# Kernel tuning notes

Hardware: AMD Instinct MI355X
Metric: run time of the kernel (lower is better)

The kernel has to match this reference:

```python
import jax, jax.numpy as jnp
import numpy as np

BS, N, XC, K, YS = 64, 1024, 1024, 256, 768

def setup_inputs() -> dict:
    key = jax.random.key(0)
    ks = jax.random.split(key, 5)
    return {
        "x": jax.random.normal(ks[0], (BS, N, XC), dtype=jnp.float32),
        "y": jax.random.normal(ks[1], (BS, YS), dtype=jnp.float32),
        "W_ch": jax.random.normal(ks[2], (K, XC), dtype=jnp.float32) * 0.02,
        "b_ch": jax.random.normal(ks[3], (K,), dtype=jnp.float32) * 0.02,
        "W_y": jax.random.normal(ks[4], (K, YS), dtype=jnp.float32) * 0.02,
    }

def reference(x, y, W_ch, b_ch, W_y):
    # y_k: [bs, k] (no bias)
    y_k = jnp.einsum('bs,ks->bk', y, W_y)
    # channel affine on every spatial position, batched: [bs, n, k]
    x_k = jnp.einsum('bnc,kc->bnk', x, W_ch) + b_ch
    # add per-sample y_k (broadcast over spatial dim), tanh, softmax over k
    z = jnp.tanh(x_k + y_k[:, None, :])
    attn = jax.nn.softmax(z, axis=-1)
    # torch.cat over dim=0 of per-sample [n, k] blocks -> [bs*n, k]
    return attn.reshape(-1, attn.shape[-1])
```

## Files before the change

kernel.cpp:

```cpp
#include <hip/hip_runtime.h>


#define XC    1024
#define KOUT  256
#define NT    16
#define LDSZ  16384

typedef float        f32x4_t  __attribute__((ext_vector_type(4)));
typedef unsigned int u32x4_t  __attribute__((ext_vector_type(4)));
typedef unsigned int u32x2_t  __attribute__((ext_vector_type(2)));
typedef __bf16       bf16x8_t __attribute__((ext_vector_type(8)));

__device__ __forceinline__ unsigned short f2bf(float f) {
  unsigned int u = __float_as_uint(f);
  u += 0x7fffu + ((u >> 16) & 1u);
  return (unsigned short)(u >> 16);
}

__device__ __forceinline__ float fast_tanh(float v) {
  float e = __expf(2.0f * v);
  return 1.0f - 2.0f / (e + 1.0f);
}

#define LGKM_BARRIER() do {                                  \
    asm volatile("s_waitcnt lgkmcnt(0)" ::: "memory");       \
    __builtin_amdgcn_s_barrier();                            \
    __builtin_amdgcn_sched_barrier(0);                       \
  } while (0)

__global__ void prep_kernel(const float* __restrict__ Wch,
                            const float* __restrict__ y,
                            const float* __restrict__ Wy,
                            const float* __restrict__ bch,
                            unsigned short* __restrict__ wbf,
                            float* __restrict__ biasws) {
  if (blockIdx.x < 256) {
    const int k = blockIdx.x;
    const int u = threadIdx.x;
    f32x4_t v = ((const f32x4_t*)(Wch + k * XC))[u];
    const int c0   = u << 2;
    const int t    = c0 >> 6;
    const int ch   = (c0 & 63) >> 3;
    const int kk   = ch >> 2;
    const int lg   = ch & 3;
    const int half = (c0 >> 2) & 1;
    const int wv   = k >> 6;
    const int ni   = (k >> 4) & 3;
    const int lr   = k & 15;
    const int lane = (lg << 4) | lr;
    unsigned int lo = (unsigned int)f2bf(v.x) | ((unsigned int)f2bf(v.y) << 16);
    unsigned int hi = (unsigned int)f2bf(v.z) | ((unsigned int)f2bf(v.w) << 16);
    char* p = (char*)wbf +
              ((size_t)((((t << 2) + wv) * 2 + kk) * 4 + ni) << 10) +
              (lane << 4) + (half << 3);
    *(u32x2_t*)p = (u32x2_t){lo, hi};
  } else {
    __shared__ __align__(16) float ys[768];
    const int b = blockIdx.x - 256;
    const int k = threadIdx.x;
    for (int i = k; i < 768; i += 256) ys[i] = y[b * 768 + i];
    __syncthreads();
    const f32x4_t* w4 = (const f32x4_t*)(Wy + k * 768);
    const f32x4_t* y4 = (const f32x4_t*)ys;
    float s = 0.f;
#pragma unroll 8
    for (int i = 0; i < 192; ++i) {
      f32x4_t w = w4[i], a = y4[i];
      s = fmaf(w.x, a.x, s); s = fmaf(w.y, a.y, s);
      s = fmaf(w.z, a.z, s); s = fmaf(w.w, a.w, s);
    }
    biasws[b * 256 + k] = s + bch[k];
  }
}

__global__ __launch_bounds__(256, 2) void fused_kernel(
    const float* __restrict__ x, const unsigned short* __restrict__ wbf,
    const float* __restrict__ bias, float* __restrict__ out) {
  __shared__ __align__(16) unsigned char smem[LDSZ];
  const int tid = threadIdx.x;
  const int l   = tid & 63;
  const int wv  = tid >> 6;
  const int lr  = l & 15;
  const int lg  = l >> 4;
  const int m0  = blockIdx.x << 6;
  const int bidx = m0 >> 10;
  const int rr  = tid >> 4;
  const int c4  = tid & 15;

  f32x4_t acc[4][4];
#pragma unroll
  for (int i = 0; i < 4; ++i)
#pragma unroll
    for (int j = 0; j < 4; ++j) acc[i][j] = (f32x4_t){0.f, 0.f, 0.f, 0.f};

  const float* xb = x + (size_t)m0 * XC + (size_t)rr * XC + (c4 << 2);
  const char* wsrc = (const char*)wbf;
  f32x4_t avA[4], avB[4];
  bf16x8_t bfr[8];

#define LOADA(dst, tt) do {                                                  \
    _Pragma("unroll")                                                        \
    for (int j = 0; j < 4; ++j)                                              \
      dst[j] = *(const f32x4_t*)(xb + (size_t)(j << 4) * XC + ((tt) << 6));  \
  } while (0)

#define LOADB(tt) do {                                                       \
    const char* g = wsrc + (size_t)(tt) * 32768 + (wv << 13) + (l << 4);     \
    _Pragma("unroll")                                                        \
    for (int f = 0; f < 8; ++f)                                              \
      bfr[f] = __builtin_bit_cast(bf16x8_t, *(const u32x4_t*)(g + (f << 10)));\
  } while (0)

#define WRITEA(src, buf) do {                                                \
    _Pragma("unroll")                                                        \
    for (int j = 0; j < 4; ++j) {                                            \
      const int row = (j << 4) + rr;                                         \
      unsigned int lo = (unsigned int)f2bf(src[j].x) |                       \
                        ((unsigned int)f2bf(src[j].y) << 16);                \
      unsigned int hi = (unsigned int)f2bf(src[j].z) |                       \
                        ((unsigned int)f2bf(src[j].w) << 16);                \
      char* p = (char*)smem + ((buf) << 13) + row * 128 +                    \
                (((c4 >> 1) ^ (row & 7)) << 4) + ((c4 & 1) << 3);            \
      *(u32x2_t*)p = (u32x2_t){lo, hi};                                      \
    }                                                                        \
  } while (0)

#define COMPUTE(buf) do {                                                    \
    const u32x4_t* aB = (const u32x4_t*)(smem + ((buf) << 13));              \
    _Pragma("unroll")                                                        \
    for (int kk = 0; kk < 2; ++kk) {                                         \
      const int cs = ((kk << 2) | lg) ^ (lr & 7);                            \
      bf16x8_t afr[4];                                                       \
      _Pragma("unroll")                                                      \
      for (int mi = 0; mi < 4; ++mi)                                         \
        afr[mi] = __builtin_bit_cast(bf16x8_t, aB[(((mi << 4) + lr) << 3) + cs]);\
      _Pragma("unroll")                                                      \
      for (int mi = 0; mi < 4; ++mi)                                         \
        _Pragma("unroll")                                                    \
        for (int nj = 0; nj < 4; ++nj)                                       \
          acc[mi][nj] = __builtin_amdgcn_mfma_f32_16x16x32_bf16(             \
              afr[mi], bfr[(kk << 2) | nj], acc[mi][nj], 0, 0, 0);           \
    }                                                                        \
  } while (0)

  LOADA(avA, 0);
  LOADA(avB, 1);
  LOADB(0);
  WRITEA(avA, 0);
  LGKM_BARRIER();

  for (int t = 0; t < NT; t += 2) {
    if (t + 2 < NT) LOADA(avA, t + 2);
    COMPUTE(0);
    if (t + 1 < NT) LOADB(t + 1);
    if (t + 1 < NT) WRITEA(avB, 1);
    LGKM_BARRIER();
    if (t + 3 < NT) LOADA(avB, t + 3);
    COMPUTE(1);
    if (t + 2 < NT) LOADB(t + 2);
    if (t + 2 < NT) WRITEA(avA, 0);
    if (t + 2 < NT) LGKM_BARRIER();
  }
  __syncthreads();

#undef LOADA
#undef LOADB
#undef WRITEA
#undef COMPUTE

  float* wred    = (float*)smem;
  float* rowstat = (float*)(smem + 1024);

  float brow[4];
#pragma unroll
  for (int ni = 0; ni < 4; ++ni)
    brow[ni] = bias[(bidx << 8) + (wv << 6) + (ni << 4) + lr];

#pragma unroll
  for (int mi = 0; mi < 4; ++mi)
#pragma unroll
    for (int ni = 0; ni < 4; ++ni)
#pragma unroll
      for (int r = 0; r < 4; ++r)
        acc[mi][ni][r] = fast_tanh(acc[mi][ni][r] + brow[ni]);

#pragma unroll
  for (int mi = 0; mi < 4; ++mi)
#pragma unroll
    for (int r = 0; r < 4; ++r) {
      float m = fmaxf(fmaxf(acc[mi][0][r], acc[mi][1][r]),
                      fmaxf(acc[mi][2][r], acc[mi][3][r]));
      m = fmaxf(m, __shfl_xor(m, 1));
      m = fmaxf(m, __shfl_xor(m, 2));
      m = fmaxf(m, __shfl_xor(m, 4));
      m = fmaxf(m, __shfl_xor(m, 8));
      if (lr == 0) wred[(wv << 6) + (mi << 4) + (lg << 2) + r] = m;
    }
  __syncthreads();
  if (tid < 64)
    rowstat[tid] = fmaxf(fmaxf(wred[tid], wred[64 + tid]),
                         fmaxf(wred[128 + tid], wred[192 + tid]));
  __syncthreads();

#pragma unroll
  for (int mi = 0; mi < 4; ++mi)
#pragma unroll
    for (int r = 0; r < 4; ++r) {
      const int row = (mi << 4) + (lg << 2) + r;
      const float m = rowstat[row];
      float s = 0.f;
#pragma unroll
      for (int ni = 0; ni < 4; ++ni) {
        float e = __expf(acc[mi][ni][r] - m);
        acc[mi][ni][r] = e;
        s += e;
      }
      s += __shfl_xor(s, 1);
      s += __shfl_xor(s, 2);
      s += __shfl_xor(s, 4);
      s += __shfl_xor(s, 8);
      if (lr == 0) wred[(wv << 6) + row] = s;
    }
  __syncthreads();
  if (tid < 64)
    rowstat[tid] = 1.0f / (wred[tid] + wred[64 + tid] +
                           wred[128 + tid] + wred[192 + tid]);
  __syncthreads();

#pragma unroll
  for (int mi = 0; mi < 4; ++mi)
#pragma unroll
    for (int r = 0; r < 4; ++r) {
      const int row = (mi << 4) + (lg << 2) + r;
      const float rinv = rowstat[row];
      float* orow = out + (size_t)(m0 + row) * KOUT + (wv << 6) + lr;
#pragma unroll
      for (int ni = 0; ni < 4; ++ni)
        orow[ni << 4] = acc[mi][ni][r] * rinv;
    }
}

extern "C" void kernel_launch(void* const* d_in, const int* in_sizes, int n_in,
                              void* d_out, int out_size, void* d_ws, size_t ws_size,
                              hipStream_t stream) {
  (void)in_sizes; (void)n_in; (void)out_size; (void)ws_size;
  const float* x   = (const float*)d_in[0];
  const float* y   = (const float*)d_in[1];
  const float* Wch = (const float*)d_in[2];
  const float* bch = (const float*)d_in[3];
  const float* Wy  = (const float*)d_in[4];
  float* out = (float*)d_out;
  unsigned short* wbf = (unsigned short*)d_ws;
  float* biasws = (float*)((char*)d_ws + 512 * 1024);

  hipLaunchKernelGGL(prep_kernel, dim3(320), dim3(256), 0, stream,
                     Wch, y, Wy, bch, wbf, biasws);
  hipLaunchKernelGGL(fused_kernel, dim3(1024), dim3(256), 0, stream,
                     x, wbf, biasws, out);
}
```

Baseline: 117.5 us.

## Stage weight tiles into LDS via async global_load_lds with triple-buffered A

```diff
diff --git a/kernel.cpp b/kernel.cpp
--- a/kernel.cpp
+++ b/kernel.cpp
@@ -4,7 +4,8 @@
 #define XC    1024
 #define KOUT  256
 #define NT    16
-#define LDSZ  16384
+#define B_OFF 16384
+#define LDSZ  81920
 
 typedef float        f32x4_t  __attribute__((ext_vector_type(4)));
 typedef unsigned int u32x4_t  __attribute__((ext_vector_type(4)));
@@ -17,16 +18,24 @@
   return (unsigned short)(u >> 16);
 }
 
+__device__ __forceinline__ unsigned int pack2bf(float a, float b) {
+  unsigned int ua = __float_as_uint(a) + 0x8000u;
+  unsigned int ub = __float_as_uint(b) + 0x8000u;
+  return (ua >> 16) | (ub & 0xffff0000u);
+}
+
 __device__ __forceinline__ float fast_tanh(float v) {
   float e = __expf(2.0f * v);
   return 1.0f - 2.0f / (e + 1.0f);
 }
 
-#define LGKM_BARRIER() do {                                  \
-    asm volatile("s_waitcnt lgkmcnt(0)" ::: "memory");       \
-    __builtin_amdgcn_s_barrier();                            \
-    __builtin_amdgcn_sched_barrier(0);                       \
-  } while (0)
+__device__ __forceinline__ void async_copy16(void* lds, const void* g) {
+  __builtin_amdgcn_global_load_lds(
+      (const __attribute__((address_space(1))) void*)g,
+      (__attribute__((address_space(3))) void*)lds, 16, 0, 0);
+}
+
+#define PIPE_WAIT(N) asm volatile("s_waitcnt vmcnt(" #N ")" ::: "memory")
 
 __global__ void prep_kernel(const float* __restrict__ Wch,
                             const float* __restrict__ y,
@@ -86,6 +95,7 @@
   const int bidx = m0 >> 10;
   const int rr  = tid >> 4;
   const int c4  = tid & 15;
+  const int t0  = blockIdx.x & 15;
 
   f32x4_t acc[4][4];
 #pragma unroll
@@ -95,8 +105,7 @@
 
   const float* xb = x + (size_t)m0 * XC + (size_t)rr * XC + (c4 << 2);
   const char* wsrc = (const char*)wbf;
-  f32x4_t avA[4], avB[4];
-  bf16x8_t bfr[8];
+  f32x4_t av0[4], av1[4], av2[4];
 
 #define LOADA(dst, tt) do {                                                  \
     _Pragma("unroll")                                                        \
@@ -104,21 +113,20 @@
       dst[j] = *(const f32x4_t*)(xb + (size_t)(j << 4) * XC + ((tt) << 6));  \
   } while (0)
 
-#define LOADB(tt) do {                                                       \
+#define DMAB(tt, buf) do {                                                   \
     const char* g = wsrc + (size_t)(tt) * 32768 + (wv << 13) + (l << 4);     \
-    _Pragma("unroll")                                                        \
-    for (int f = 0; f < 8; ++f)                                              \
-      bfr[f] = __builtin_bit_cast(bf16x8_t, *(const u32x4_t*)(g + (f << 10)));\
+    unsigned char* d = smem + B_OFF + ((buf) << 15) + (wv << 13);            \
+    _Pragma("unroll")                                                        \
+    for (int i = 0; i < 8; ++i)                                              \
+      async_copy16(d + (i << 10), g + (i << 10));                            \
   } while (0)
 
 #define WRITEA(src, buf) do {                                                \
     _Pragma("unroll")                                                        \
     for (int j = 0; j < 4; ++j) {                                            \
       const int row = (j << 4) + rr;                                         \
-      unsigned int lo = (unsigned int)f2bf(src[j].x) |                       \
-                        ((unsigned int)f2bf(src[j].y) << 16);                \
-      unsigned int hi = (unsigned int)f2bf(src[j].z) |                       \
-                        ((unsigned int)f2bf(src[j].w) << 16);                \
+      unsigned int lo = pack2bf(src[j].x, src[j].y);                         \
+      unsigned int hi = pack2bf(src[j].z, src[j].w);                         \
       char* p = (char*)smem + ((buf) << 13) + row * 128 +                    \
                 (((c4 >> 1) ^ (row & 7)) << 4) + ((c4 & 1) << 3);            \
       *(u32x2_t*)p = (u32x2_t){lo, hi};                                      \
@@ -127,46 +135,73 @@
 
 #define COMPUTE(buf) do {                                                    \
     const u32x4_t* aB = (const u32x4_t*)(smem + ((buf) << 13));              \
+    const u32x4_t* bB = (const u32x4_t*)(smem + B_OFF + ((buf) << 15));      \
     _Pragma("unroll")                                                        \
     for (int kk = 0; kk < 2; ++kk) {                                         \
       const int cs = ((kk << 2) | lg) ^ (lr & 7);                            \
-      bf16x8_t afr[4];                                                       \
+      bf16x8_t afr[4], bfr[4];                                               \
       _Pragma("unroll")                                                      \
       for (int mi = 0; mi < 4; ++mi)                                         \
         afr[mi] = __builtin_bit_cast(bf16x8_t, aB[(((mi << 4) + lr) << 3) + cs]);\
+      _Pragma("unroll")                                                      \
+      for (int nj = 0; nj < 4; ++nj)                                         \
+        bfr[nj] = __builtin_bit_cast(bf16x8_t,                               \
+            bB[((((wv << 3) + (kk << 2) + nj)) << 6) + l]);                  \
       _Pragma("unroll")                                                      \
       for (int mi = 0; mi < 4; ++mi)                                         \
         _Pragma("unroll")                                                    \
         for (int nj = 0; nj < 4; ++nj)                                       \
           acc[mi][nj] = __builtin_amdgcn_mfma_f32_16x16x32_bf16(             \
-              afr[mi], bfr[(kk << 2) | nj], acc[mi][nj], 0, 0, 0);           \
+              afr[mi], bfr[nj], acc[mi][nj], 0, 0, 0);                       \
     }                                                                        \
   } while (0)
 
-  LOADA(avA, 0);
-  LOADA(avB, 1);
-  LOADB(0);
-  WRITEA(avA, 0);
-  LGKM_BARRIER();
-
-  for (int t = 0; t < NT; t += 2) {
-    if (t + 2 < NT) LOADA(avA, t + 2);
-    COMPUTE(0);
-    if (t + 1 < NT) LOADB(t + 1);
-    if (t + 1 < NT) WRITEA(avB, 1);
-    LGKM_BARRIER();
-    if (t + 3 < NT) LOADA(avB, t + 3);
-    COMPUTE(1);
-    if (t + 2 < NT) LOADB(t + 2);
-    if (t + 2 < NT) WRITEA(avA, 0);
-    if (t + 2 < NT) LGKM_BARRIER();
-  }
+#define STEP(s, aW, aL, VM) do {                                             \
+    if ((s) + 1 < NT) DMAB((((s) + 1 + t0) & 15), ((s) + 1) & 1);            \
+    if ((s) + 3 < NT) LOADA(aL, (((s) + 3 + t0) & 15));                      \
+    COMPUTE((s) & 1);                                                        \
+    if ((s) + 1 < NT) {                                                      \
+      WRITEA(aW, ((s) + 1) & 1);                                             \
+      asm volatile("s_waitcnt lgkmcnt(0)" ::: "memory");                     \
+      PIPE_WAIT(VM);                                                         \
+      __builtin_amdgcn_s_barrier();                                          \
+      __builtin_amdgcn_sched_barrier(0);                                     \
+    }                                                                        \
+  } while (0)
+
+  DMAB(t0, 0);
+  LOADA(av0, t0);
+  LOADA(av1, (t0 + 1) & 15);
+  LOADA(av2, (t0 + 2) & 15);
+  WRITEA(av0, 0);
+  asm volatile("s_waitcnt lgkmcnt(0)" ::: "memory");
+  __builtin_amdgcn_s_barrier();
+  __builtin_amdgcn_sched_barrier(0);
+
+  STEP( 0, av1, av0, 4);
+  STEP( 1, av2, av1, 4);
+  STEP( 2, av0, av2, 4);
+  STEP( 3, av1, av0, 4);
+  STEP( 4, av2, av1, 4);
+  STEP( 5, av0, av2, 4);
+  STEP( 6, av1, av0, 4);
+  STEP( 7, av2, av1, 4);
+  STEP( 8, av0, av2, 4);
+  STEP( 9, av1, av0, 4);
+  STEP(10, av2, av1, 4);
+  STEP(11, av0, av2, 4);
+  STEP(12, av1, av0, 4);
+  STEP(13, av2, av1, 0);
+  STEP(14, av0, av0, 0);
+  STEP(15, av0, av0, 0);
+
   __syncthreads();
 
 #undef LOADA
-#undef LOADB
+#undef DMAB
 #undef WRITEA
 #undef COMPUTE
+#undef STEP
 
   float* wred    = (float*)smem;
   float* rowstat = (float*)(smem + 1024);
```

Result: no change. 118.8 us (+1.1%).
